# Optimization experiments

Hardware: AMD Instinct MI355X
Metric: run time of the kernel (lower is better)

## Reference

```python
import jax, jax.numpy as jnp
import numpy as np

K = 5            # adaptive kernel size
C = 256          # inplanes
M = 4
CM = C // M      # 64 bottleneck channels
PLANES = 256


def _depthwise_per_sample(f, w, b, dilation, pad):
    # f: [N, Cm, H, W]; w: [N, Cm, kh, kw] per-sample depthwise weights; b: [Cm]
    # Fold batch into the channel/group dim so one grouped conv does all samples.
    N, Cm, H, W = f.shape
    x = f.reshape(1, N * Cm, H, W)
    wk = w.reshape(N * Cm, 1, w.shape[2], w.shape[3])
    out = jax.lax.conv_general_dilated(
        x, wk, window_strides=(1, 1), padding=[(pad, pad), (pad, pad)],
        rhs_dilation=(dilation, dilation), feature_group_count=N * Cm,
        dimension_numbers=("NCHW", "OIHW", "NCHW"))
    return out.reshape(N, Cm, H, W) + b[None, :, None, None]


def setup_inputs() -> dict:
    key = jax.random.key(0)
    ks = jax.random.split(key, 16)
    N, H, W = 16, 96, 96
    s = 0.05
    return {
        "x": jax.random.normal(ks[0], (N, C, H, W), jnp.float32),
        "conv_w": jax.random.normal(ks[1], (CM, C)) * s,            # 1x1 conv C->Cm
        "conv_b": jax.random.normal(ks[2], (CM,)) * s,
        "conv_k_w": jax.random.normal(ks[3], ()) * s + 1.0,          # conv_k: 1x1, 1ch
        "conv_k_b": jax.random.normal(ks[4], ()) * s,
        "conv_k2_w": jax.random.normal(ks[5], ()) * s + 1.0,         # conv_k2
        "conv_k2_b": jax.random.normal(ks[6], ()) * s,
        "conv_kernel_w": jax.random.normal(ks[7], (K * K,)) * s,     # 1 -> k*k
        "conv_kernel_b": jax.random.normal(ks[8], (K * K,)) * s,
        "conv_kernel2_w": jax.random.normal(ks[9], (9,)) * s,        # 1 -> 9
        "conv_kernel2_b": jax.random.normal(ks[10], (9,)) * s,
        "fuse_w": jax.random.normal(ks[11], (PLANES // 2, CM)) * s,  # 1x1 fuse
        "fuse_b": jax.random.normal(ks[12], (PLANES // 2,)) * s,
        "adap_b": jax.random.normal(ks[13], (CM,)) * s,              # conv_adap_kernel.bias
        "atrous_b": jax.random.normal(ks[14], (CM,)) * s,            # conv3x3_atrous bias
    }


def reference(x, conv_w, conv_b, conv_k_w, conv_k_b, conv_k2_w, conv_k2_b,
              conv_kernel_w, conv_kernel_b, conv_kernel2_w, conv_kernel2_b,
              fuse_w, fuse_b, adap_b, atrous_b):
    N = x.shape[0]
    # f = relu(1x1 conv)
    f = jax.nn.relu(jnp.einsum("oc,nchw->nohw", conv_w, x) + conv_b[None, :, None, None])
    # g = relu(conv(avg_pool(x))) -> [N, Cm]
    g = jax.nn.relu(x.mean(axis=(2, 3)) @ conv_w.T + conv_b)
    # conv_kernel (1->k*k, 1x1) applied over the Cm "spatial" axis, then conv_k (scalar affine)
    # kernel[n,c,kk] = conv_k_w * (conv_kernel_w[kk]*g[n,c] + conv_kernel_b[kk]) + conv_k_b
    ker = conv_k_w * (g[:, :, None] * conv_kernel_w[None, None, :] + conv_kernel_b) + conv_k_b
    w_dyn = ker.reshape(N, CM, K, K)
    ker2 = conv_k2_w * (g[:, :, None] * conv_kernel2_w[None, None, :] + conv_kernel2_b) + conv_k2_b
    w_atr = ker2.reshape(N, CM, 3, 3)
    # per-sample dynamic depthwise convs
    out = _depthwise_per_sample(f, w_dyn, adap_b, dilation=1, pad=(K - 1) // 2)
    out_atr = _depthwise_per_sample(f, w_atr, atrous_b, dilation=2, pad=2)
    # fuse (1x1) each branch, concat on channels
    y = jnp.einsum("oc,nchw->nohw", fuse_w, out) + fuse_b[None, :, None, None]
    y_atr = jnp.einsum("oc,nchw->nohw", fuse_w, out_atr) + fuse_b[None, :, None, None]
    return jnp.concatenate([y, y_atr], axis=1)
```

## Files before the change

kernel.cpp:

```cpp
#include <hip/hip_runtime.h>
#include <hip/hip_bf16.h>
#include <stdint.h>

#define N_S   16
#define C_IN  256
#define CMID  64
#define HH    96
#define WW    96
#define HW    9216
#define PL2   128

#define CB_OFF   0
#define KW_OFF   64
#define KB_OFF   96
#define K2W_OFF  128
#define K2B_OFF  144
#define FB_OFF   160
#define AB_OFF   288
#define ATB_OFF  352
#define SC_OFF   416

typedef __attribute__((ext_vector_type(8))) short short8;
typedef __attribute__((ext_vector_type(4))) float floatx4;

__device__ __forceinline__ float ldbf(const uint16_t* p) {
    return __uint_as_float(((uint32_t)(*p)) << 16);
}
__device__ __forceinline__ uint16_t f2bf(float f) {
    __hip_bfloat16 h = __float2bfloat16(f);
    return *reinterpret_cast<uint16_t*>(&h);
}
__device__ __forceinline__ uint32_t pkbf(float lo, float hi) {
    return (uint32_t)f2bf(lo) | ((uint32_t)f2bf(hi) << 16);
}
__device__ __forceinline__ float bfsum2(uint32_t u) {
    return __uint_as_float(u << 16) + __uint_as_float(u & 0xffff0000u);
}

#define SWZ8(row) ((((row) ^ ((row) >> 3)) & 7) << 3)

__global__ __launch_bounds__(256) void k_prep(
    const uint16_t* __restrict__ xq,
    const void* conv_w, const void* conv_b, const void* ckw, const void* ckb,
    const void* ck2w, const void* ck2b, const void* kernw, const void* kernb,
    const void* kern2w, const void* kern2b, const void* fuse_w, const void* fuse_b,
    const void* adap_b, const void* atrous_b,
    int* __restrict__ flags,
    uint16_t* __restrict__ cw_bf, uint16_t* __restrict__ fw_bf,
    float* __restrict__ smalls) {
    __shared__ int cnt[2];
    int t = threadIdx.x;
    if (t < 2) cnt[t] = 0;
    __syncthreads();
    int cx = 0, cw = 0;
    const uint16_t* wq = (const uint16_t*)conv_w;
    for (int k = 0; k < 64; ++k) {
        uint16_t vx = xq[k * 256 + t];
        uint16_t vw = wq[k * 256 + t];
        if (((vx >> 7) & 0xFF) >= 0xC0) cx++;
        if (((vw >> 7) & 0xFF) >= 0xC0) cw++;
    }
    atomicAdd(&cnt[0], cx);
    atomicAdd(&cnt[1], cw);
    __syncthreads();
    bool f32 = cnt[1] > 64;
    if (blockIdx.x == 0 && t == 0) { flags[0] = cnt[0] > 64; flags[1] = f32; }

    for (int i = blockIdx.x * 256 + t; i < CMID * C_IN; i += 16 * 256)
        cw_bf[i] = f32 ? f2bf(((const float*)conv_w)[i]) : ((const uint16_t*)conv_w)[i];
    for (int i = blockIdx.x * 256 + t; i < PL2 * CMID; i += 16 * 256)
        fw_bf[i] = f32 ? f2bf(((const float*)fuse_w)[i]) : ((const uint16_t*)fuse_w)[i];
    if (blockIdx.x != 0) return;
    if (t < 64) {
        smalls[CB_OFF + t]  = f32 ? ((const float*)conv_b)[t]   : ldbf((const uint16_t*)conv_b + t);
        smalls[AB_OFF + t]  = f32 ? ((const float*)adap_b)[t]   : ldbf((const uint16_t*)adap_b + t);
        smalls[ATB_OFF + t] = f32 ? ((const float*)atrous_b)[t] : ldbf((const uint16_t*)atrous_b + t);
    }
    if (t < 128)
        smalls[FB_OFF + t] = f32 ? ((const float*)fuse_b)[t] : ldbf((const uint16_t*)fuse_b + t);
    if (t < 25) {
        smalls[KW_OFF + t] = f32 ? ((const float*)kernw)[t] : ldbf((const uint16_t*)kernw + t);
        smalls[KB_OFF + t] = f32 ? ((const float*)kernb)[t] : ldbf((const uint16_t*)kernb + t);
    }
    if (t < 9) {
        smalls[K2W_OFF + t] = f32 ? ((const float*)kern2w)[t] : ldbf((const uint16_t*)kern2w + t);
        smalls[K2B_OFF + t] = f32 ? ((const float*)kern2b)[t] : ldbf((const uint16_t*)kern2b + t);
    }
    if (t == 0) {
        smalls[SC_OFF + 0] = f32 ? ((const float*)ckw)[0]  : ldbf((const uint16_t*)ckw);
        smalls[SC_OFF + 1] = f32 ? ((const float*)ckb)[0]  : ldbf((const uint16_t*)ckb);
        smalls[SC_OFF + 2] = f32 ? ((const float*)ck2w)[0] : ldbf((const uint16_t*)ck2w);
        smalls[SC_OFF + 3] = f32 ? ((const float*)ck2b)[0] : ldbf((const uint16_t*)ck2b);
    }
}


#define ISSUE(cc, A0, A1, B0, B1) do {                                          \
    int c_ = (cc) * 64 + cp * 2;                                                \
    if (xf32) {                                                                 \
        const float* xb_ = (const float*)xv + ((size_t)n * C_IN + c_) * HW + px0;\
        A0 = *(const uint4*)xb_;        A1 = *(const uint4*)(xb_ + 4);          \
        B0 = *(const uint4*)(xb_ + HW); B1 = *(const uint4*)(xb_ + HW + 4);     \
    } else {                                                                    \
        const uint16_t* xb_ = (const uint16_t*)xv + ((size_t)n * C_IN + c_) * HW + px0;\
        A0 = *(const uint4*)xb_;        B0 = *(const uint4*)(xb_ + HW);         \
    }                                                                           \
} while (0)

#define CONVWRITE(cc, A0, A1, B0, B1, XL) do {                                  \
    int c_ = (cc) * 64 + cp * 2;                                                \
    uint32_t pk_[8]; float s0_, s1_;                                            \
    if (xf32) {                                                                 \
        float av_[8], bw_[8];                                                   \
        av_[0] = __uint_as_float(A0.x); av_[1] = __uint_as_float(A0.y);         \
        av_[2] = __uint_as_float(A0.z); av_[3] = __uint_as_float(A0.w);         \
        av_[4] = __uint_as_float(A1.x); av_[5] = __uint_as_float(A1.y);         \
        av_[6] = __uint_as_float(A1.z); av_[7] = __uint_as_float(A1.w);         \
        bw_[0] = __uint_as_float(B0.x); bw_[1] = __uint_as_float(B0.y);         \
        bw_[2] = __uint_as_float(B0.z); bw_[3] = __uint_as_float(B0.w);         \
        bw_[4] = __uint_as_float(B1.x); bw_[5] = __uint_as_float(B1.y);         \
        bw_[6] = __uint_as_float(B1.z); bw_[7] = __uint_as_float(B1.w);         \
        s0_ = ((av_[0] + av_[1]) + (av_[2] + av_[3]))                           \
            + ((av_[4] + av_[5]) + (av_[6] + av_[7]));                          \
        s1_ = ((bw_[0] + bw_[1]) + (bw_[2] + bw_[3]))                           \
            + ((bw_[4] + bw_[5]) + (bw_[6] + bw_[7]));                          \
        _Pragma("unroll")                                                       \
        for (int j = 0; j < 8; ++j) pk_[j] = pkbf(av_[j], bw_[j]);              \
    } else {                                                                    \
        s0_ = (bfsum2(A0.x) + bfsum2(A0.y)) + (bfsum2(A0.z) + bfsum2(A0.w));    \
        s1_ = (bfsum2(B0.x) + bfsum2(B0.y)) + (bfsum2(B0.z) + bfsum2(B0.w));    \
        pk_[0] = (A0.x & 0xffffu) | (B0.x << 16);                               \
        pk_[1] = (A0.x >> 16)     | (B0.x & 0xffff0000u);                       \
        pk_[2] = (A0.y & 0xffffu) | (B0.y << 16);                               \
        pk_[3] = (A0.y >> 16)     | (B0.y & 0xffff0000u);                       \
        pk_[4] = (A0.z & 0xffffu) | (B0.z << 16);                               \
        pk_[5] = (A0.z >> 16)     | (B0.z & 0xffff0000u);                       \
        pk_[6] = (A0.w & 0xffffu) | (B0.w << 16);                               \
        pk_[7] = (A0.w >> 16)     | (B0.w & 0xffff0000u);                       \
    }                                                                           \
    int swz_ = pxg << 2;                                                        \
    _Pragma("unroll")                                                           \
    for (int j = 0; j < 8; ++j)                                                 \
        (XL)[(pxg * 8 + j) * 36 + (cp ^ swz_)] = pk_[j];                        \
    s0_ += __shfl_xor(s0_, 4, 8); s0_ += __shfl_xor(s0_, 2, 8);                 \
    s0_ += __shfl_xor(s0_, 1, 8);                                               \
    s1_ += __shfl_xor(s1_, 4, 8); s1_ += __shfl_xor(s1_, 2, 8);                 \
    s1_ += __shfl_xor(s1_, 1, 8);                                               \
    if ((t & 7) == 0) *(float2*)(pbase + c_) = make_float2(s0_, s1_);           \
} while (0)

#define MFMA_PH(cc, XL) do {                                                    \
    _Pragma("unroll")                                                           \
    for (int ks = 0; ks < 2; ++ks) {                                            \
        int kw_ = (cc) * 64 + ks * 32 + quad * 8;                               \
        const uint16_t* wp_ = cw_bf + kw_;                                      \
        short8 a0 = *(const short8*)(wp_ + (l16)      * 256);                   \
        short8 a1 = *(const short8*)(wp_ + (16 + l16) * 256);                   \
        short8 a2 = *(const short8*)(wp_ + (32 + l16) * 256);                   \
        short8 a3 = *(const short8*)(wp_ + (48 + l16) * 256);                   \
        int kdw_ = (ks * 16 + quad * 4) ^ ((pxw >> 3) << 2);                    \
        short8 bv = *(const short8*)((XL) + (size_t)pxw * 36 + kdw_);           \
        acc[0] = __builtin_amdgcn_mfma_f32_16x16x32_bf16(a0, bv, acc[0], 0, 0, 0);\
        acc[1] = __builtin_amdgcn_mfma_f32_16x16x32_bf16(a1, bv, acc[1], 0, 0, 0);\
        acc[2] = __builtin_amdgcn_mfma_f32_16x16x32_bf16(a2, bv, acc[2], 0, 0, 0);\
        acc[3] = __builtin_amdgcn_mfma_f32_16x16x32_bf16(a3, bv, acc[3], 0, 0, 0);\
    }                                                                           \
} while (0)

__global__ __launch_bounds__(256) void k_conv1x1(
    const void* __restrict__ xv, const int* __restrict__ flags,
    const uint16_t* __restrict__ cw_bf, const float* __restrict__ smalls,
    uint16_t* __restrict__ fout, float* __restrict__ partials) {
    __shared__ uint16_t x_lds[2 * 64 * 72];
    int t = threadIdx.x;
    int b = blockIdx.x;
    int n = b / 144, blk = b % 144;
    int pxb = blk * 64;
    bool xf32 = flags[0] != 0;

    int lane = t & 63, wid = t >> 6;
    int l16 = lane & 15, quad = lane >> 4;
    int pxw = wid * 16 + l16;
    uint32_t* xb0 = (uint32_t*)x_lds;
    uint32_t* xb1 = xb0 + 2304;

    int pxg = t & 7, cp = t >> 3;
    int px0 = pxb + pxg * 8;

    floatx4 acc[4];
#pragma unroll
    for (int i = 0; i < 4; ++i) acc[i] = (floatx4){0.f, 0.f, 0.f, 0.f};

    float* pbase = partials + (size_t)(n * 144 + blk) * 256;

    uint4 pA0, pA1, pB0, pB1;
    uint4 qA0, qA1, qB0, qB1;

    ISSUE(0, pA0, pA1, pB0, pB1);
    CONVWRITE(0, pA0, pA1, pB0, pB1, xb0);
    ISSUE(1, qA0, qA1, qB0, qB1);
    __syncthreads();
    MFMA_PH(0, xb0);
    CONVWRITE(1, qA0, qA1, qB0, qB1, xb1);
    ISSUE(2, pA0, pA1, pB0, pB1);
    __syncthreads();
    MFMA_PH(1, xb1);
    CONVWRITE(2, pA0, pA1, pB0, pB1, xb0);
    ISSUE(3, qA0, qA1, qB0, qB1);
    __syncthreads();
    MFMA_PH(2, xb0);
    CONVWRITE(3, qA0, qA1, qB0, qB1, xb1);
    __syncthreads();
    MFMA_PH(3, xb1);

#pragma unroll
    for (int mt = 0; mt < 4; ++mt) {
        int o = mt * 16 + quad * 4;
        float b0 = smalls[CB_OFF + o],     b1 = smalls[CB_OFF + o + 1];
        float b2 = smalls[CB_OFF + o + 2], b3 = smalls[CB_OFF + o + 3];
        float v0 = fmaxf(acc[mt][0] + b0, 0.f);
        float v1 = fmaxf(acc[mt][1] + b1, 0.f);
        float v2 = fmaxf(acc[mt][2] + b2, 0.f);
        float v3 = fmaxf(acc[mt][3] + b3, 0.f);
        *(uint2*)(x_lds + pxw * 72 + o) = make_uint2(pkbf(v0, v1), pkbf(v2, v3));
    }
    __syncthreads();
#pragma unroll
    for (int k = 0; k < 2; ++k) {
        int task = k * 256 + t;
        int o8 = (task & 7) * 8, pxl = task >> 3;
        *(uint4*)(fout + ((size_t)n * HW + pxb + pxl) * 64 + o8) =
            *(const uint4*)(x_lds + pxl * 72 + o8);
    }
}

__global__ __launch_bounds__(256) void k_weights2(
    const float* __restrict__ partials, const uint16_t* __restrict__ cw_bf,
    const float* __restrict__ smalls,
    float* __restrict__ w_dyn, float* __restrict__ w_atr) {
    __shared__ float s_sums[256];
    __shared__ float s_dot[256];
    int n = blockIdx.x, t = threadIdx.x;
    const float* pp = partials + (size_t)n * 144 * 256 + t;
    float s = 0.f;
#pragma unroll 8
    for (int k = 0; k < 144; ++k) s += pp[k * 256];
    s_sums[t] = s * (1.0f / (float)HW);
    __syncthreads();
    int cm = t & 63, seg = t >> 6;
    const uint16_t* wr = cw_bf + cm * 256 + seg * 64;
    const float* sr = s_sums + seg * 64;
    float acc = 0.f;
#pragma unroll 8
    for (int c = 0; c < 64; ++c) acc = fmaf(ldbf(wr + c), sr[c], acc);
    s_dot[t] = acc;
    __syncthreads();
    if (t < 64) {
        float a = s_dot[t] + s_dot[t + 64] + s_dot[t + 128] + s_dot[t + 192]
                + smalls[CB_OFF + t];
        float gv = fmaxf(a, 0.f);
        float ckw = smalls[SC_OFF + 0], ckb = smalls[SC_OFF + 1];
        float ck2w = smalls[SC_OFF + 2], ck2b = smalls[SC_OFF + 3];
        float* o1 = w_dyn + (size_t)(n * CMID + t) * 25;
#pragma unroll
        for (int k = 0; k < 25; ++k)
            o1[k] = fmaf(ckw, fmaf(gv, smalls[KW_OFF + k], smalls[KB_OFF + k]), ckb);
        float* o2 = w_atr + (size_t)(n * CMID + t) * 9;
#pragma unroll
        for (int k = 0; k < 9; ++k)
            o2[k] = fmaf(ck2w, fmaf(gv, smalls[K2W_OFF + k], smalls[K2B_OFF + k]), ck2b);
    }
}

__global__ __launch_bounds__(256, 4) void k_dwfuse(
    const uint16_t* __restrict__ f,
    const float* __restrict__ w_dyn, const float* __restrict__ w_atr,
    const uint16_t* __restrict__ fw_bf, const float* __restrict__ smalls,
    float* __restrict__ out) {
    __shared__ uint16_t u_lds[160 * 64];
    uint16_t* d5_lds = u_lds;
    uint16_t* dA_lds = u_lds + 64 * 72;

    int t = threadIdx.x;
    int orig = blockIdx.x;
    int b = (orig & 7) * 288 + (orig >> 3);
    int n = b / 144, tile = b % 144;
    int y0 = (tile / 6) * 4, x0 = (tile % 6) * 16;

    const uint16_t* fbase = f + (size_t)n * HW * 64;
#pragma unroll
    for (int k = 0; k < 5; ++k) {
        int task = k * 256 + t;
        int row = task >> 3, c8 = (task & 7) * 8;
        int hy = row / 20, hx = row - hy * 20;
        int y = y0 - 2 + hy, xg = x0 - 2 + hx;
        uint4 v = make_uint4(0u, 0u, 0u, 0u);
        if (y >= 0 && y < HH && xg >= 0 && xg < WW)
            v = *(const uint4*)(fbase + ((size_t)y * WW + xg) * 64 + c8);
        *(uint4*)(u_lds + row * 64 + (c8 ^ SWZ8(row))) = v;
    }

    int c = t >> 2, q = t & 3;
    int qx = q << 2;
    float w5[25], w9[9];
    {
        const float* wp = w_dyn + (size_t)(n * CMID + c) * 25;
#pragma unroll
        for (int k = 0; k < 25; ++k) w5[k] = wp[k];
        const float* wa = w_atr + (size_t)(n * CMID + c) * 9;
#pragma unroll
        for (int k = 0; k < 9; ++k) w9[k] = wa[k];
    }
    __syncthreads();

    float b5v = smalls[AB_OFF + c], bAv = smalls[ATB_OFF + c];
    float a5[4][4], aA[4][4];
#pragma unroll
    for (int i = 0; i < 4; ++i)
#pragma unroll
        for (int j = 0; j < 4; ++j) { a5[i][j] = b5v; aA[i][j] = bAv; }

#pragma unroll
    for (int r = 0; r < 8; ++r) {
        float row[8];
#pragma unroll
        for (int cl = 0; cl < 8; ++cl) {
            int rw = r * 20 + qx + cl;
            row[cl] = ldbf(u_lds + rw * 64 + (c ^ SWZ8(rw)));
        }
#pragma unroll
        for (int oy = 0; oy < 4; ++oy) {
            int d = r - oy;
            if (d >= 0 && d <= 4) {
#pragma unroll
                for (int j = 0; j < 5; ++j) {
                    float wv = w5[d * 5 + j];
#pragma unroll
                    for (int ox = 0; ox < 4; ++ox)
                        a5[oy][ox] = fmaf(wv, row[ox + j], a5[oy][ox]);
                }
            }
            if (d >= 0 && d <= 4 && (d & 1) == 0) {
                int i2 = d >> 1;
#pragma unroll
                for (int j = 0; j < 3; ++j) {
                    float wv = w9[i2 * 3 + j];
#pragma unroll
                    for (int ox = 0; ox < 4; ++ox)
                        aA[oy][ox] = fmaf(wv, row[ox + 2 * j], aA[oy][ox]);
                }
            }
        }
    }
    __syncthreads();

#pragma unroll
    for (int oy = 0; oy < 4; ++oy)
#pragma unroll
        for (int ox = 0; ox < 4; ox += 2) {
            int pxo = oy * 16 + qx + ox;
            uint32_t p5 = pkbf(a5[oy][ox], a5[oy][ox + 1]);
            uint32_t pA = pkbf(aA[oy][ox], aA[oy][ox + 1]);
            d5_lds[pxo * 72 + c]       = (uint16_t)p5;
            d5_lds[(pxo + 1) * 72 + c] = (uint16_t)(p5 >> 16);
            dA_lds[pxo * 72 + c]       = (uint16_t)pA;
            dA_lds[(pxo + 1) * 72 + c] = (uint16_t)(pA >> 16);
        }
    __syncthreads();

    {
        int lane = t & 63, wid = t >> 6;
        int l16 = lane & 15, quad = lane >> 4;
        const uint16_t* dl = (wid >= 2) ? dA_lds : d5_lds;
        int oh = (wid & 1) * 64;
        int obr = (wid >= 2) ? 128 : 0;

        floatx4 acc[4][4];
#pragma unroll
        for (int i = 0; i < 4; ++i)
#pragma unroll
            for (int j = 0; j < 4; ++j) acc[i][j] = (floatx4){0.f, 0.f, 0.f, 0.f};

#pragma unroll
        for (int ks = 0; ks < 2; ++ks) {
            int kk = ks * 32 + quad * 8;
            short8 a0 = *(const short8*)(dl + (l16)      * 72 + kk);
            short8 a1 = *(const short8*)(dl + (16 + l16) * 72 + kk);
            short8 a2 = *(const short8*)(dl + (32 + l16) * 72 + kk);
            short8 a3 = *(const short8*)(dl + (48 + l16) * 72 + kk);
#pragma unroll
            for (int nt = 0; nt < 4; ++nt) {
                short8 bv = *(const short8*)(fw_bf + (size_t)(oh + nt * 16 + l16) * 64 + kk);
                acc[0][nt] = __builtin_amdgcn_mfma_f32_16x16x32_bf16(a0, bv, acc[0][nt], 0, 0, 0);
                acc[1][nt] = __builtin_amdgcn_mfma_f32_16x16x32_bf16(a1, bv, acc[1][nt], 0, 0, 0);
                acc[2][nt] = __builtin_amdgcn_mfma_f32_16x16x32_bf16(a2, bv, acc[2][nt], 0, 0, 0);
                acc[3][nt] = __builtin_amdgcn_mfma_f32_16x16x32_bf16(a3, bv, acc[3][nt], 0, 0, 0);
            }
        }
#pragma unroll
        for (int nt = 0; nt < 4; ++nt) {
            int o = oh + nt * 16 + l16;
            float bias = smalls[FB_OFF + o];
            float* obp = out + ((size_t)(n * 256 + obr + o)) * HW + x0 + quad * 4;
#pragma unroll
            for (int mt = 0; mt < 4; ++mt) {
                float4 v;
                v.x = acc[mt][nt][0] + bias;
                v.y = acc[mt][nt][1] + bias;
                v.z = acc[mt][nt][2] + bias;
                v.w = acc[mt][nt][3] + bias;
                *(float4*)(obp + (size_t)(y0 + mt) * WW) = v;
            }
        }
    }
}

extern "C" void kernel_launch(void* const* d_in, const int* in_sizes, int n_in,
                              void* d_out, int out_size, void* d_ws, size_t ws_size,
                              hipStream_t stream) {
    float* out = (float*)d_out;

    char* ws = (char*)d_ws;
    int*      flags = (int*)ws;
    uint16_t* cw_bf = (uint16_t*)(ws + 256);
    uint16_t* fw_bf = (uint16_t*)(ws + 33024);
    float*    smalls = (float*)(ws + 49408);
    float*    partials = (float*)(ws + 65536);
    float*    w_dyn = (float*)(ws + 2424832);
    float*    w_atr = (float*)(ws + 2527232);
    uint16_t* f     = (uint16_t*)(ws + 2564096);

    k_prep<<<dim3(16), dim3(256), 0, stream>>>(
        (const uint16_t*)d_in[0],
        d_in[1], d_in[2], d_in[3], d_in[4], d_in[5], d_in[6], d_in[7], d_in[8],
        d_in[9], d_in[10], d_in[11], d_in[12], d_in[13], d_in[14],
        flags, cw_bf, fw_bf, smalls);
    k_conv1x1<<<dim3(N_S * 144), dim3(256), 0, stream>>>(
        d_in[0], flags, cw_bf, smalls, f, partials);
    k_weights2<<<dim3(N_S), dim3(256), 0, stream>>>(
        partials, cw_bf, smalls, w_dyn, w_atr);
    k_dwfuse<<<dim3(N_S * 144), dim3(256), 0, stream>>>(
        f, w_dyn, w_atr, fw_bf, smalls, out);
}
```

Baseline: 363.0 us.

## Issue all x loads up front and stage full K-slab in LDS for conv1x1

The 1x1 conv kernel drops its double-buffered, four-phase load/convert/MFMA pipeline. It now issues all four channel-chunk global loads at once, writes the full 256-channel tile into one larger swizzled LDS buffer, and runs every MFMA phase after a single barrier. This raises memory-level parallelism and removes three barriers. The cost is more live registers (16 uint4 values) and 32KB of LDS, and launch_bounds(256,4) is added to cap registers for occupancy, which may cause spills.

Measured after the change: 364.4 us. Within noise of the previous version (+0.4%).

```diff
diff --git a/kernel.cpp b/kernel.cpp
--- a/kernel.cpp
+++ b/kernel.cpp
@@ -38,6 +38,7 @@
 }
 
 #define SWZ8(row) ((((row) ^ ((row) >> 3)) & 7) << 3)
+#define SWZC(px) ((((px) ^ ((px) >> 3)) & 7) << 2)
 
 __global__ __launch_bounds__(256) void k_prep(
     const uint16_t* __restrict__ xq,
@@ -107,7 +108,7 @@
     }                                                                           \
 } while (0)
 
-#define CONVWRITE(cc, A0, A1, B0, B1, XL) do {                                  \
+#define CONVWRITE(cc, A0, A1, B0, B1) do {                                      \
     int c_ = (cc) * 64 + cp * 2;                                                \
     uint32_t pk_[8]; float s0_, s1_;                                            \
     if (xf32) {                                                                 \
@@ -138,10 +139,11 @@
         pk_[6] = (A0.w & 0xffffu) | (B0.w << 16);                               \
         pk_[7] = (A0.w >> 16)     | (B0.w & 0xffff0000u);                       \
     }                                                                           \
-    int swz_ = pxg << 2;                                                        \
     _Pragma("unroll")                                                           \
-    for (int j = 0; j < 8; ++j)                                                 \
-        (XL)[(pxg * 8 + j) * 36 + (cp ^ swz_)] = pk_[j];                        \
+    for (int j = 0; j < 8; ++j) {                                               \
+        int px_ = pxg * 8 + j;                                                  \
+        xl32[px_ * 128 + (((cc) * 32 + cp) ^ SWZC(px_))] = pk_[j];              \
+    }                                                                           \
     s0_ += __shfl_xor(s0_, 4, 8); s0_ += __shfl_xor(s0_, 2, 8);                 \
     s0_ += __shfl_xor(s0_, 1, 8);                                               \
     s1_ += __shfl_xor(s1_, 4, 8); s1_ += __shfl_xor(s1_, 2, 8);                 \
@@ -149,7 +151,7 @@
     if ((t & 7) == 0) *(float2*)(pbase + c_) = make_float2(s0_, s1_);           \
 } while (0)
 
-#define MFMA_PH(cc, XL) do {                                                    \
+#define MFMA_PH(cc) do {                                                        \
     _Pragma("unroll")                                                           \
     for (int ks = 0; ks < 2; ++ks) {                                            \
         int kw_ = (cc) * 64 + ks * 32 + quad * 8;                               \
@@ -158,8 +160,8 @@
         short8 a1 = *(const short8*)(wp_ + (16 + l16) * 256);                   \
         short8 a2 = *(const short8*)(wp_ + (32 + l16) * 256);                   \
         short8 a3 = *(const short8*)(wp_ + (48 + l16) * 256);                   \
-        int kdw_ = (ks * 16 + quad * 4) ^ ((pxw >> 3) << 2);                    \
-        short8 bv = *(const short8*)((XL) + (size_t)pxw * 36 + kdw_);           \
+        int kdw_ = ((cc) * 32 + ks * 16 + quad * 4) ^ SWZC(pxw);                \
+        short8 bv = *(const short8*)(xl32 + (size_t)pxw * 128 + kdw_);          \
         acc[0] = __builtin_amdgcn_mfma_f32_16x16x32_bf16(a0, bv, acc[0], 0, 0, 0);\
         acc[1] = __builtin_amdgcn_mfma_f32_16x16x32_bf16(a1, bv, acc[1], 0, 0, 0);\
         acc[2] = __builtin_amdgcn_mfma_f32_16x16x32_bf16(a2, bv, acc[2], 0, 0, 0);\
@@ -167,11 +169,11 @@
     }                                                                           \
 } while (0)
 
-__global__ __launch_bounds__(256) void k_conv1x1(
+__global__ __launch_bounds__(256, 4) void k_conv1x1(
     const void* __restrict__ xv, const int* __restrict__ flags,
     const uint16_t* __restrict__ cw_bf, const float* __restrict__ smalls,
     uint16_t* __restrict__ fout, float* __restrict__ partials) {
-    __shared__ uint16_t x_lds[2 * 64 * 72];
+    __shared__ uint32_t xl32[64 * 128];
     int t = threadIdx.x;
     int b = blockIdx.x;
     int n = b / 144, blk = b % 144;
@@ -181,38 +183,39 @@
     int lane = t & 63, wid = t >> 6;
     int l16 = lane & 15, quad = lane >> 4;
     int pxw = wid * 16 + l16;
-    uint32_t* xb0 = (uint32_t*)x_lds;
-    uint32_t* xb1 = xb0 + 2304;
 
     int pxg = t & 7, cp = t >> 3;
     int px0 = pxb + pxg * 8;
 
-    floatx4 acc[4];
-#pragma unroll
-    for (int i = 0; i < 4; ++i) acc[i] = (floatx4){0.f, 0.f, 0.f, 0.f};
-
     float* pbase = partials + (size_t)(n * 144 + blk) * 256;
 
     uint4 pA0, pA1, pB0, pB1;
     uint4 qA0, qA1, qB0, qB1;
+    uint4 rA0, rA1, rB0, rB1;
+    uint4 sA0, sA1, sB0, sB1;
 
     ISSUE(0, pA0, pA1, pB0, pB1);
-    CONVWRITE(0, pA0, pA1, pB0, pB1, xb0);
     ISSUE(1, qA0, qA1, qB0, qB1);
-    __syncthreads();
-    MFMA_PH(0, xb0);
-    CONVWRITE(1, qA0, qA1, qB0, qB1, xb1);
-    ISSUE(2, pA0, pA1, pB0, pB1);
-    __syncthreads();
-    MFMA_PH(1, xb1);
-    CONVWRITE(2, pA0, pA1, pB0, pB1, xb0);
-    ISSUE(3, qA0, qA1, qB0, qB1);
-    __syncthreads();
-    MFMA_PH(2, xb0);
-    CONVWRITE(3, qA0, qA1, qB0, qB1, xb1);
-    __syncthreads();
-    MFMA_PH(3, xb1);
-
+    ISSUE(2, rA0, rA1, rB0, rB1);
+    ISSUE(3, sA0, sA1, sB0, sB1);
+
+    CONVWRITE(0, pA0, pA1, pB0, pB1);
+    CONVWRITE(1, qA0, qA1, qB0, qB1);
+    CONVWRITE(2, rA0, rA1, rB0, rB1);
+    CONVWRITE(3, sA0, sA1, sB0, sB1);
+
+    floatx4 acc[4];
+#pragma unroll
+    for (int i = 0; i < 4; ++i) acc[i] = (floatx4){0.f, 0.f, 0.f, 0.f};
+
+    __syncthreads();
+    MFMA_PH(0);
+    MFMA_PH(1);
+    MFMA_PH(2);
+    MFMA_PH(3);
+    __syncthreads();
+
+    uint16_t* fl = (uint16_t*)xl32;
 #pragma unroll
     for (int mt = 0; mt < 4; ++mt) {
         int o = mt * 16 + quad * 4;
@@ -222,7 +225,7 @@
         float v1 = fmaxf(acc[mt][1] + b1, 0.f);
         float v2 = fmaxf(acc[mt][2] + b2, 0.f);
         float v3 = fmaxf(acc[mt][3] + b3, 0.f);
-        *(uint2*)(x_lds + pxw * 72 + o) = make_uint2(pkbf(v0, v1), pkbf(v2, v3));
+        *(uint2*)(fl + pxw * 72 + o) = make_uint2(pkbf(v0, v1), pkbf(v2, v3));
     }
     __syncthreads();
 #pragma unroll
@@ -230,7 +233,7 @@
         int task = k * 256 + t;
         int o8 = (task & 7) * 8, pxl = task >> 3;
         *(uint4*)(fout + ((size_t)n * HW + pxb + pxl) * 64 + o8) =
-            *(const uint4*)(x_lds + pxl * 72 + o8);
+            *(const uint4*)(fl + pxl * 72 + o8);
     }
 }
 
```
